# Kernel optimization log

Measured on AMD Instinct MI355X. Metric: run time of the kernel, lower is better.

## Reference

```python
import jax, jax.numpy as jnp
import numpy as np

B, L, D, H = 4, 4096, 1024, 16
DH = D // H  # 64


def setup_inputs() -> dict:
    key = jax.random.key(0)
    k1, k2, k3, k4 = jax.random.split(key, 4)
    x = jax.random.normal(k1, (B, L, D), dtype=jnp.float32)
    # torch.nn.Linear weights stored as [out_features, in_features]
    Wq = jax.random.normal(k2, (D, D), dtype=jnp.float32) * 0.02
    Wkv = jax.random.normal(k3, (2 * D, D), dtype=jnp.float32) * 0.02
    Wout = jax.random.normal(k4, (D, D), dtype=jnp.float32) * 0.02
    return {"x": x, "Wq": Wq, "Wkv": Wkv, "Wout": Wout}


def reference(x, Wq, Wkv, Wout):
    b, l, d = x.shape
    # q: (B, L, H, Dh) -- NOTE: source never transposes to (B,H,L,Dh)
    q = (x @ Wq.T).reshape(b, l, H, DH)
    kv = (x @ Wkv.T).reshape(b, l, H, 2, DH)
    k = kv[..., 0, :]  # (B, L, H, Dh)
    v = kv[..., 1, :]  # (B, L, H, Dh)
    # Faithful to source: matmul over the last two dims -> (B, L, H, H)
    # i.e. attention over the HEAD axis at each (b, l) position.
    attn = jnp.einsum('blhd,bljd->blhj', q, k) / jnp.sqrt(jnp.float32(DH))
    attn = jax.nn.softmax(attn, axis=-1)
    out = jnp.einsum('blhj,bljd->blhd', attn, v).reshape(b, l, d)
    return out @ Wout.T
```

## Files before the change

kernel.cpp:

```cpp
#include <hip/hip_runtime.h>

typedef unsigned short ushort_t;
typedef __attribute__((ext_vector_type(8))) __bf16 bf16x8;
typedef __attribute__((ext_vector_type(4))) float f32x4;

#define NB 4
#define NL 4096
#define ND 1024
#define NH 16
#define NDH 64
#define NM (NB*NL)

__device__ __forceinline__ ushort_t f2bf(float f) {
  unsigned u = __builtin_bit_cast(unsigned, f);
  u += 0x7fffu + ((u >> 16) & 1u);
  return (ushort_t)(u >> 16);
}

__device__ __forceinline__ void gl_lds16(const void* g, void* l) {
  __builtin_amdgcn_global_load_lds(
      (const __attribute__((address_space(1))) unsigned*)g,
      (__attribute__((address_space(3))) unsigned*)l, 16, 0, 0);
}

__global__ __launch_bounds__(256) void k_cvt4(
    const float* __restrict__ x, const float* __restrict__ Wq,
    const float* __restrict__ Wkv, const float* __restrict__ Wout,
    ushort_t* __restrict__ xb, ushort_t* __restrict__ Wcat,
    ushort_t* __restrict__ Woutb)
{
  int i = blockIdx.x * 256 + threadIdx.x;
  const int stride = gridDim.x * 256;
  for (; i < 5242880; i += stride) {
    const float4* src; ushort4* dst; int off;
    if (i < 4194304)      { src = (const float4*)x;    dst = (ushort4*)xb;                 off = i; }
    else if (i < 4456448) { src = (const float4*)Wq;   dst = (ushort4*)Wcat;               off = i - 4194304; }
    else if (i < 4980736) { src = (const float4*)Wkv;  dst = (ushort4*)(Wcat + 1048576);   off = i - 4456448; }
    else                  { src = (const float4*)Wout; dst = (ushort4*)Woutb;              off = i - 4980736; }
    float4 v = src[off];
    ushort4 o;
    o.x = f2bf(v.x); o.y = f2bf(v.y); o.z = f2bf(v.z); o.w = f2bf(v.w);
    dst[off] = o;
  }
}

template<int MODE>
__global__ __launch_bounds__(512, 2) void k_gemm256(
    const ushort_t* __restrict__ A, const ushort_t* __restrict__ Bt,
    void* __restrict__ Cout, int N, int gridN)
{
  __shared__ __align__(16) ushort_t As[2][16384];
  __shared__ __align__(16) ushort_t Bs[2][16384];
  constexpr int K = 1024;
  const int tid = threadIdx.x;
  const int lane = tid & 63, wv = tid >> 6;
  const int wm = wv >> 2, wn = wv & 3;
  const int l15 = lane & 15, lhi = lane >> 4;

  const int nb = gridDim.x * gridDim.y;
  const int lid = blockIdx.y * gridDim.x + blockIdx.x;
  const int perx = nb >> 3;
  const int xcd = lid & 7, l = lid >> 3;
  const int stC = gridN >> 2;
  const int st = l >> 4, wi = l & 15;
  const int rp = xcd * (perx / gridN) + (st / stC) * 4 + (wi >> 2);
  const int cp = (st % stC) * 4 + (wi & 3);
  const int rowBase = rp * 256;
  const int colBase = cp * 256;

  const ushort_t* Abase = A + (size_t)rowBase * K;
  const ushort_t* Bbase = Bt + (size_t)colBase * K;

  const int so = tid >> 3;
  const int scol = (tid & 7) * 8;
  const int ssw = (so & 7) << 3;
  int offA[2][2], offB[2][2];
#pragma unroll
  for (int r = 0; r < 2; ++r)
#pragma unroll
    for (int k = 0; k < 2; ++k) {
      int slot = r*128 + k*64 + so;
      int rowA = ((slot & 64) << 1) | ((slot & 128) >> 1) | (slot & 63);
      int rowB = (((slot >> 5) & 3) << 6) | (((slot >> 7) & 1) << 5) | (slot & 31);
      offA[r][k] = rowA * K + (scol ^ ssw);
      offB[r][k] = rowB * K + (scol ^ ssw);
    }
  const int sbase = wv * 512;

#define STAGE_A(dst, R, KT) do { \
  gl_lds16(Abase + offA[R][0] + (KT)*64, &As[dst][(R)*8192 + sbase]); \
  gl_lds16(Abase + offA[R][1] + (KT)*64, &As[dst][(R)*8192 + 4096 + sbase]); \
} while(0)
#define STAGE_B(dst, R, KT) do { \
  gl_lds16(Bbase + offB[R][0] + (KT)*64, &Bs[dst][(R)*8192 + sbase]); \
  gl_lds16(Bbase + offB[R][1] + (KT)*64, &Bs[dst][(R)*8192 + 4096 + sbase]); \
} while(0)

  const int fsw = (l15 & 7) << 3;
  const int kc0 = (lhi * 8) ^ fsw;
  const int kc1 = (32 + lhi * 8) ^ fsw;

  f32x4 acc[8][4] = {};

#define PHASE(CUR, QM, QN, STAGEOP) do { \
  const ushort_t* Ap = &As[CUR][((QM)*128 + wm*64 + l15)*64]; \
  const ushort_t* Bp = &Bs[CUR][((QN)*128 + wn*32 + l15)*64]; \
  bf16x8 af[4][2], bfr[2][2]; \
  _Pragma("unroll") for (int i_ = 0; i_ < 4; ++i_) { \
    af[i_][0] = *(const bf16x8*)&Ap[i_*1024 + kc0]; \
    af[i_][1] = *(const bf16x8*)&Ap[i_*1024 + kc1]; } \
  _Pragma("unroll") for (int j_ = 0; j_ < 2; ++j_) { \
    bfr[j_][0] = *(const bf16x8*)&Bp[j_*1024 + kc0]; \
    bfr[j_][1] = *(const bf16x8*)&Bp[j_*1024 + kc1]; } \
  STAGEOP; \
  __builtin_amdgcn_s_barrier(); \
  __builtin_amdgcn_s_setprio(1); \
  _Pragma("unroll") for (int i_ = 0; i_ < 4; ++i_) \
  _Pragma("unroll") for (int j_ = 0; j_ < 2; ++j_) { \
    acc[(QM)*4+i_][(QN)*2+j_] = __builtin_amdgcn_mfma_f32_16x16x32_bf16(af[i_][0], bfr[j_][0], acc[(QM)*4+i_][(QN)*2+j_], 0, 0, 0); \
    acc[(QM)*4+i_][(QN)*2+j_] = __builtin_amdgcn_mfma_f32_16x16x32_bf16(af[i_][1], bfr[j_][1], acc[(QM)*4+i_][(QN)*2+j_], 0, 0, 0); } \
  __builtin_amdgcn_s_setprio(0); \
  __builtin_amdgcn_s_barrier(); \
} while(0)

  STAGE_A(0, 0, 0); STAGE_B(0, 0, 0); STAGE_A(0, 1, 0); STAGE_B(0, 1, 0);
  STAGE_A(1, 0, 1); STAGE_B(1, 0, 1);
  asm volatile("s_waitcnt vmcnt(4)" ::: "memory");
  __builtin_amdgcn_s_barrier();

  for (int t = 0; t < 16; ++t) {
    const int cur = t & 1;
    const int nxt = cur ^ 1;
    const bool s1 = (t < 15), s2 = (t < 14);
    PHASE(cur, 0, 0, if (s1) STAGE_A(nxt, 1, t + 1));
    PHASE(cur, 0, 1, if (s1) STAGE_B(nxt, 1, t + 1));
    PHASE(cur, 1, 0, if (s2) STAGE_A(cur, 0, t + 2));
    PHASE(cur, 1, 1, if (s2) STAGE_B(cur, 0, t + 2));
    if (t < 14) asm volatile("s_waitcnt vmcnt(4)" ::: "memory");
    else        asm volatile("s_waitcnt vmcnt(0)" ::: "memory");
    __builtin_amdgcn_s_barrier();
  }
#undef PHASE
#undef STAGE_A
#undef STAGE_B

  const int orow = rowBase + wm * 128 + lhi * 4;
  const int ocol = colBase + wn * 64 + l15;
#pragma unroll
  for (int i = 0; i < 8; ++i)
#pragma unroll
    for (int j = 0; j < 4; ++j)
#pragma unroll
      for (int rr = 0; rr < 4; ++rr) {
        int gr = orow + i * 16 + rr;
        int gc = ocol + j * 16;
        if (MODE == 2) ((float*)Cout)[(size_t)gr * N + gc] = acc[i][j][rr];
        else           ((ushort_t*)Cout)[(size_t)gr * N + gc] = f2bf(acc[i][j][rr]);
      }
}

__global__ __launch_bounds__(256) void k_attn(
    const ushort_t* __restrict__ qkv, ushort_t* __restrict__ aout)
{
  __shared__ __align__(16) ushort_t qs[4][16*72];
  __shared__ __align__(16) ushort_t kvs[4][16*136];
  __shared__ __align__(16) ushort_t ps[4][16*40];
  __shared__ __align__(16) ushort_t os[4][1024];
  const int tid = threadIdx.x, lane = tid & 63, wave = tid >> 6;
  const int t = blockIdx.x * 4 + wave;
  const int l15 = lane & 15, lhi = lane >> 4;
  const ushort_t* row = qkv + (size_t)t * 3072;

#pragma unroll
  for (int c = 0; c < 6; ++c) {
    int c8 = c * 64 + lane;
    bf16x8 v = *(const bf16x8*)(row + c8 * 8);
    if (c8 < 128) {
      int h = c8 >> 3, off = (c8 & 7) * 8;
      *(bf16x8*)&qs[wave][h*72 + off] = v;
    } else {
      int e = c8 * 8 - 1024;
      int h = e >> 7, off = e & 127;
      *(bf16x8*)&kvs[wave][h*136 + off] = v;
    }
  }
  if (lane < 16) {
    bf16x8 z = {};
    *(bf16x8*)&ps[wave][lane*40 + 16] = z;
    *(bf16x8*)&ps[wave][lane*40 + 24] = z;
  }
  __syncthreads();

  bf16x8 aq0 = *(const bf16x8*)&qs[wave][l15*72 + lhi*8];
  bf16x8 aq1 = *(const bf16x8*)&qs[wave][l15*72 + 32 + lhi*8];
  bf16x8 bk0 = *(const bf16x8*)&kvs[wave][l15*136 + lhi*8];
  bf16x8 bk1 = *(const bf16x8*)&kvs[wave][l15*136 + 32 + lhi*8];
  f32x4 s = {};
  s = __builtin_amdgcn_mfma_f32_16x16x32_bf16(aq0, bk0, s, 0, 0, 0);
  s = __builtin_amdgcn_mfma_f32_16x16x32_bf16(aq1, bk1, s, 0, 0, 0);

#pragma unroll
  for (int r = 0; r < 4; ++r) {
    float sv = s[r] * 0.125f;
    float tm = sv;
#pragma unroll
    for (int off = 1; off < 16; off <<= 1) tm = fmaxf(tm, __shfl_xor(tm, off, 64));
    float p = __expf(sv - tm);
    float rs = p;
#pragma unroll
    for (int off = 1; off < 16; off <<= 1) rs += __shfl_xor(rs, off, 64);
    p /= rs;
    ps[wave][(lhi*4 + r)*40 + l15] = f2bf(p);
  }
  __syncthreads();

  bf16x8 pa = *(const bf16x8*)&ps[wave][l15*40 + lhi*8];
#pragma unroll
  for (int dt = 0; dt < 4; ++dt) {
    bf16x8 vb;
#pragma unroll
    for (int i = 0; i < 8; ++i) {
      int j = (lhi*8 + i) & 15;
      vb[i] = __builtin_bit_cast(__bf16, kvs[wave][j*136 + 64 + dt*16 + l15]);
    }
    f32x4 o = {};
    o = __builtin_amdgcn_mfma_f32_16x16x32_bf16(pa, vb, o, 0, 0, 0);
#pragma unroll
    for (int r = 0; r < 4; ++r)
      os[wave][(lhi*4 + r)*64 + dt*16 + l15] = f2bf(o[r]);
  }
  __syncthreads();

  ushort_t* orow = aout + (size_t)t * 1024;
#pragma unroll
  for (int c = 0; c < 2; ++c) {
    int idx = (c*64 + lane) * 8;
    *(bf16x8*)(orow + idx) = *(const bf16x8*)&os[wave][idx];
  }
}

extern "C" void kernel_launch(void* const* d_in, const int* in_sizes, int n_in,
                              void* d_out, int out_size, void* d_ws, size_t ws_size,
                              hipStream_t stream) {
  const float* x    = (const float*)d_in[0];
  const float* Wq   = (const float*)d_in[1];
  const float* Wkv  = (const float*)d_in[2];
  const float* Wout = (const float*)d_in[3];
  float* out = (float*)d_out;

  ushort_t* ws    = (ushort_t*)d_ws;
  ushort_t* xb    = ws;
  ushort_t* Wcat  = xb + 16777216;
  ushort_t* Woutb = Wcat + 3145728;
  ushort_t* qkv   = Woutb + 1048576;
  ushort_t* aout  = xb;

  k_cvt4<<<2048, 256, 0, stream>>>(x, Wq, Wkv, Wout, xb, Wcat, Woutb);

  dim3 g1(12, 64);
  k_gemm256<0><<<g1, 512, 0, stream>>>(xb, Wcat, qkv, 3072, 12);

  k_attn<<<NM/4, 256, 0, stream>>>(qkv, aout);

  dim3 g3(4, 64);
  k_gemm256<2><<<g3, 512, 0, stream>>>(aout, Woutb, out, 1024, 4);
}
```

Measured before the change: 223.5 us.

## Simplify GEMM mainloop to full-tile double buffering with one barrier per step

Replaces the four-phase quadrant pipeline, which staged partial tiles two steps ahead with per-phase barriers, with plain double buffering. Each step prefetches the whole next K tile, computes two K-halves across all fragments, then waits for all loads and synchronizes once. The LDS row mapping and the global offsets are simplified to a linear layout. This removes many barriers and waitcnt points, at the risk of exposing global load latency at the end of each step.

```diff
diff --git a/kernel.cpp b/kernel.cpp
--- a/kernel.cpp
+++ b/kernel.cpp
@@ -74,26 +74,20 @@
   const int so = tid >> 3;
   const int scol = (tid & 7) * 8;
   const int ssw = (so & 7) << 3;
-  int offA[2][2], offB[2][2];
-#pragma unroll
-  for (int r = 0; r < 2; ++r)
-#pragma unroll
-    for (int k = 0; k < 2; ++k) {
-      int slot = r*128 + k*64 + so;
-      int rowA = ((slot & 64) << 1) | ((slot & 128) >> 1) | (slot & 63);
-      int rowB = (((slot >> 5) & 3) << 6) | (((slot >> 7) & 1) << 5) | (slot & 31);
-      offA[r][k] = rowA * K + (scol ^ ssw);
-      offB[r][k] = rowB * K + (scol ^ ssw);
-    }
+  const int offG = so * K + (scol ^ ssw);
   const int sbase = wv * 512;
 
-#define STAGE_A(dst, R, KT) do { \
-  gl_lds16(Abase + offA[R][0] + (KT)*64, &As[dst][(R)*8192 + sbase]); \
-  gl_lds16(Abase + offA[R][1] + (KT)*64, &As[dst][(R)*8192 + 4096 + sbase]); \
-} while(0)
-#define STAGE_B(dst, R, KT) do { \
-  gl_lds16(Bbase + offB[R][0] + (KT)*64, &Bs[dst][(R)*8192 + sbase]); \
-  gl_lds16(Bbase + offB[R][1] + (KT)*64, &Bs[dst][(R)*8192 + 4096 + sbase]); \
+#define STAGE(dst, KT) do { \
+  const ushort_t* Ag = Abase + (KT)*64 + offG; \
+  const ushort_t* Bg = Bbase + (KT)*64 + offG; \
+  gl_lds16(Ag,          &As[dst][sbase]); \
+  gl_lds16(Ag + 65536,  &As[dst][4096  + sbase]); \
+  gl_lds16(Ag + 131072, &As[dst][8192  + sbase]); \
+  gl_lds16(Ag + 196608, &As[dst][12288 + sbase]); \
+  gl_lds16(Bg,          &Bs[dst][sbase]); \
+  gl_lds16(Bg + 65536,  &Bs[dst][4096  + sbase]); \
+  gl_lds16(Bg + 131072, &Bs[dst][8192  + sbase]); \
+  gl_lds16(Bg + 196608, &Bs[dst][12288 + sbase]); \
 } while(0)
 
   const int fsw = (l15 & 7) << 3;
@@ -102,47 +96,36 @@
 
   f32x4 acc[8][4] = {};
 
-#define PHASE(CUR, QM, QN, STAGEOP) do { \
-  const ushort_t* Ap = &As[CUR][((QM)*128 + wm*64 + l15)*64]; \
-  const ushort_t* Bp = &Bs[CUR][((QN)*128 + wn*32 + l15)*64]; \
-  bf16x8 af[4][2], bfr[2][2]; \
-  _Pragma("unroll") for (int i_ = 0; i_ < 4; ++i_) { \
-    af[i_][0] = *(const bf16x8*)&Ap[i_*1024 + kc0]; \
-    af[i_][1] = *(const bf16x8*)&Ap[i_*1024 + kc1]; } \
-  _Pragma("unroll") for (int j_ = 0; j_ < 2; ++j_) { \
-    bfr[j_][0] = *(const bf16x8*)&Bp[j_*1024 + kc0]; \
-    bfr[j_][1] = *(const bf16x8*)&Bp[j_*1024 + kc1]; } \
-  STAGEOP; \
-  __builtin_amdgcn_s_barrier(); \
+#define HALF(CUR, KC) do { \
+  bf16x8 af[8], bfr[4]; \
+  _Pragma("unroll") for (int i_ = 0; i_ < 8; ++i_) \
+    af[i_] = *(const bf16x8*)&As[CUR][(wm*128 + i_*16 + l15)*64 + (KC)]; \
+  _Pragma("unroll") for (int j_ = 0; j_ < 4; ++j_) \
+    bfr[j_] = *(const bf16x8*)&Bs[CUR][(wn*64 + j_*16 + l15)*64 + (KC)]; \
+  __builtin_amdgcn_sched_barrier(0); \
   __builtin_amdgcn_s_setprio(1); \
-  _Pragma("unroll") for (int i_ = 0; i_ < 4; ++i_) \
-  _Pragma("unroll") for (int j_ = 0; j_ < 2; ++j_) { \
-    acc[(QM)*4+i_][(QN)*2+j_] = __builtin_amdgcn_mfma_f32_16x16x32_bf16(af[i_][0], bfr[j_][0], acc[(QM)*4+i_][(QN)*2+j_], 0, 0, 0); \
-    acc[(QM)*4+i_][(QN)*2+j_] = __builtin_amdgcn_mfma_f32_16x16x32_bf16(af[i_][1], bfr[j_][1], acc[(QM)*4+i_][(QN)*2+j_], 0, 0, 0); } \
+  _Pragma("unroll") for (int i_ = 0; i_ < 8; ++i_) \
+  _Pragma("unroll") for (int j_ = 0; j_ < 4; ++j_) \
+    acc[i_][j_] = __builtin_amdgcn_mfma_f32_16x16x32_bf16(af[i_], bfr[j_], acc[i_][j_], 0, 0, 0); \
   __builtin_amdgcn_s_setprio(0); \
-  __builtin_amdgcn_s_barrier(); \
 } while(0)
 
-  STAGE_A(0, 0, 0); STAGE_B(0, 0, 0); STAGE_A(0, 1, 0); STAGE_B(0, 1, 0);
-  STAGE_A(1, 0, 1); STAGE_B(1, 0, 1);
-  asm volatile("s_waitcnt vmcnt(4)" ::: "memory");
+  STAGE(0, 0);
+  asm volatile("s_waitcnt vmcnt(0)" ::: "memory");
   __builtin_amdgcn_s_barrier();
 
   for (int t = 0; t < 16; ++t) {
     const int cur = t & 1;
-    const int nxt = cur ^ 1;
-    const bool s1 = (t < 15), s2 = (t < 14);
-    PHASE(cur, 0, 0, if (s1) STAGE_A(nxt, 1, t + 1));
-    PHASE(cur, 0, 1, if (s1) STAGE_B(nxt, 1, t + 1));
-    PHASE(cur, 1, 0, if (s2) STAGE_A(cur, 0, t + 2));
-    PHASE(cur, 1, 1, if (s2) STAGE_B(cur, 0, t + 2));
-    if (t < 14) asm volatile("s_waitcnt vmcnt(4)" ::: "memory");
-    else        asm volatile("s_waitcnt vmcnt(0)" ::: "memory");
-    __builtin_amdgcn_s_barrier();
-  }
-#undef PHASE
-#undef STAGE_A
-#undef STAGE_B
+    if (t < 15) STAGE(cur ^ 1, t + 1);
+    HALF(cur, kc0);
+    HALF(cur, kc1);
+    if (t < 15) {
+      asm volatile("s_waitcnt vmcnt(0)" ::: "memory");
+      __builtin_amdgcn_s_barrier();
+    }
+  }
+#undef HALF
+#undef STAGE
 
   const int orow = rowBase + wm * 128 + lhi * 4;
   const int ocol = colBase + wn * 64 + l15;
```

New measurement: 192.8 us, median of 2. 13.7% less time.
